# Performance work log

Hardware: AMD Instinct MI355X
Metric: run time of the kernel (lower is better)

## Reference

```python
import jax, jax.numpy as jnp
import numpy as np

B, T, DIM = 2, 2048, 1024
HEADS, DH = 16, 64
INNER = HEADS * DH
R, ALPHA = 8, 2.0
LORA_SCALE = ALPHA / R
NUM_PATCHES, NUM_FRAMES = 256, 8  # T = NUM_PATCHES*NUM_FRAMES
EPS = 1e-5


def _block_causal_mask():
    # generate_mask_matrix: frame-block causal mask [1,1,T,T]
    f = jnp.arange(T) // NUM_PATCHES
    m = (f[:, None] >= f[None, :]).astype(jnp.int32)
    return m[None, None]


def setup_inputs() -> dict:
    key = jax.random.key(0)
    ks = jax.random.split(key, 24)
    p = lambda k, shape: (jax.random.normal(k, shape, jnp.float32) * 0.02)
    inp = {
        "x": jax.random.normal(ks[0], (B, T, DIM), jnp.float32),
        "m_tok": jax.random.normal(ks[1], (B, T, DIM), jnp.float32),
        "norm_g": jnp.ones((DIM,), jnp.float32),
        "norm_b": jnp.zeros((DIM,), jnp.float32),
        "mnorm_g": jnp.ones((DIM,), jnp.float32),
        "mnorm_b": jnp.zeros((DIM,), jnp.float32),
        # q/k/v: base W [inner,dim], LoRA A [r,dim], B [inner,r], generator G [r,dim]
        "Wq": p(ks[2], (INNER, DIM)), "Aq": p(ks[3], (R, DIM)), "Bq": p(ks[4], (INNER, R)), "Gq": p(ks[5], (R, DIM)),
        "Wk": p(ks[6], (INNER, DIM)), "Ak": p(ks[7], (R, DIM)), "Bk": p(ks[8], (INNER, R)), "Gk": p(ks[9], (R, DIM)),
        "Wv": p(ks[10], (INNER, DIM)), "Av": p(ks[11], (R, DIM)), "Bv": p(ks[12], (INNER, R)), "Gv": p(ks[13], (R, DIM)),
        # o: in=inner, out=dim, mem_features=dim
        "Wo": p(ks[14], (DIM, INNER)), "Ao": p(ks[15], (R, INNER)), "Bo": p(ks[16], (DIM, R)), "Go": p(ks[17], (R, DIM)),
        "mask": _block_causal_mask(),
    }
    return inp


def _ln(x, g, b):
    mu = jnp.mean(x, -1, keepdims=True)
    var = jnp.mean(jnp.square(x - mu), -1, keepdims=True)
    return (x - mu) * jax.lax.rsqrt(var + EPS) * g + b


def _dyn_lora(x, m, W, A, Bm, G):
    # per-token dynamic LoRA: base Wx + (alpha/r) * B @ ((A x) * (G m))
    base = jnp.einsum('btd,od->bto', x, W)
    gate = jnp.einsum('btm,rm->btr', m, G)   # per-token r-dim modulation from memory token
    low = jnp.einsum('btd,rd->btr', x, A) * gate
    return base + LORA_SCALE * jnp.einsum('btr,or->bto', low, Bm)


def reference(x, m_tok, norm_g, norm_b, mnorm_g, mnorm_b,
              Wq, Aq, Bq, Gq, Wk, Ak, Bk, Gk, Wv, Av, Bv, Gv,
              Wo, Ao, Bo, Go, mask):
    xn = _ln(x, norm_g, norm_b)
    mn = _ln(m_tok, mnorm_g, mnorm_b)
    q = _dyn_lora(xn, mn, Wq, Aq, Bq, Gq).reshape(B, T, HEADS, DH)
    k = _dyn_lora(xn, mn, Wk, Ak, Bk, Gk).reshape(B, T, HEADS, DH)
    v = _dyn_lora(xn, mn, Wv, Av, Bv, Gv).reshape(B, T, HEADS, DH)
    scale = DH ** -0.5
    dots = jnp.einsum('bihd,bjhd->bhij', q, k) * scale
    dots = jnp.where(mask[:, :, :T, :T] == 0, -jnp.inf, dots)
    attn = jax.nn.softmax(dots, axis=-1)
    out = jnp.einsum('bhij,bjhd->bihd', attn, v).reshape(B, T, INNER)
    return _dyn_lora(out, mn, Wo, Ao, Bo, Go)
```

## Files before the change

### kernel.cpp

```cpp
#include <hip/hip_runtime.h>
#include <hip/hip_bf16.h>
#include <stdint.h>

typedef __bf16 bf16;
typedef bf16 bfx4 __attribute__((ext_vector_type(4)));
typedef bf16 bfx8 __attribute__((ext_vector_type(8)));
typedef __attribute__((ext_vector_type(8))) short frag_t;
typedef __attribute__((ext_vector_type(4))) float f32x4;

#define NTOK 4096
#define LORA_SCALE_F 0.25f

#define TM 128
#define TN 64

__device__ __forceinline__ bool probe_bf16(const void* ng) {
  return *(const uint32_t*)ng == 0x3F803F80u;
}
__device__ __forceinline__ float4 load4(const void* p, int idx4, bool bf) {
  if (bf) {
    bfx4 v = ((const bfx4*)p)[idx4];
    return make_float4((float)v[0], (float)v[1], (float)v[2], (float)v[3]);
  }
  return ((const float4*)p)[idx4];
}
__device__ __forceinline__ float loadf(const void* p, int i, bool bf) {
  return bf ? (float)((const bf16*)p)[i] : ((const float*)p)[i];
}

__device__ __forceinline__ int mask_type(const void* m) {
  const uint32_t w = *(const uint32_t*)m;
  if (w == 0x3F800000u) return 1;
  if (w == 0x3F803F80u) return 2;
  return 0;
}
__device__ __forceinline__ bool mask_on(const void* m, size_t idx, int mt) {
  if (mt == 0) return ((const int*)m)[idx] != 0;
  if (mt == 1) return ((const float*)m)[idx] != 0.f;
  return ((const uint16_t*)m)[idx] != 0;
}

__device__ __forceinline__ uint32_t pkbf(float a, float b) {
  union { bf16 h; unsigned short u; } x, y;
  x.h = (bf16)a; y.h = (bf16)b;
  return (uint32_t)x.u | ((uint32_t)y.u << 16);
}

__global__ __launch_bounds__(256) void verify_kernel(const void* x, const void* mt, const void* ng,
                                                     const void* Wq, const void* mask, float* flag) {
  __shared__ int sc[3];
  const int tid = threadIdx.x;
  if (tid < 3) sc[tid] = 0;
  __syncthreads();
  const bool bf = probe_bf16(ng);
  int lx = 0, lm = 0, lw = 0;
  for (int i = tid; i < 1024; i += 256) {
    if (__builtin_fabsf(loadf(x, i, bf)) > 0.25f) lx++;
    if (__builtin_fabsf(loadf(mt, i, bf)) > 0.25f) lm++;
    if (__builtin_fabsf(loadf(Wq, i, bf)) > 0.25f) lw++;
  }
  if (lx) atomicAdd(&sc[0], lx);
  if (lm) atomicAdd(&sc[1], lm);
  if (lw) atomicAdd(&sc[2], lw);
  __syncthreads();
  if (tid != 0) return;
  int code = 0;
  const uint32_t w0 = *(const uint32_t*)mask;
  int mtp = -1;
  if (w0 == 1u) mtp = 0;
  else if (w0 == 0x3F800000u) mtp = 1;
  else if (w0 == 0x3F803F80u) mtp = 2;
  if (mtp < 0) code = 30;
  if (!code && mask_on(mask, 2047, mtp)) code = 35;
  if (!code && !mask_on(mask, (size_t)2047 * 2048, mtp)) code = 36;
  if (!code) {
    for (int i = 0; i < 8 && !code; ++i) {
      uint32_t w = ((const uint32_t*)ng)[i];
      if (bf ? (w != 0x3F803F80u) : (w != 0x3F800000u)) code = 31;
    }
  }
  if (!code) {
    if (sc[0] < 600) code = 32;
    else if (sc[1] < 600) code = 33;
    else if (sc[2] > 0) code = 34;
  }
  *flag = (float)code;
}

__global__ __launch_bounds__(256) void maskchk_kernel(const void* mask, float* flag) {
  const int mt = mask_type(mask);
  const int i = blockIdx.x;
  bool bad = false;
  for (int j = threadIdx.x; j < 2048; j += 256) {
    const bool on = mask_on(mask, (size_t)i * 2048 + j, mt);
    const bool expect = (i >> 8) >= (j >> 8);
    if (on != expect) bad = true;
  }
  if (bad) *flag = 37.f;
}

__global__ void setflag_kernel(float* flag, float v) {
  if (threadIdx.x == 0 && blockIdx.x == 0) *flag = v;
}

__global__ __launch_bounds__(256) void finalize_kernel(const float* flag, float* out, int n) {
  const float f = *flag;
  if (f == 0.f) return;
  int i = (blockIdx.x * 256 + threadIdx.x) * 4;
  if (i + 3 < n) { out[i] = f; out[i + 1] = f; out[i + 2] = f; out[i + 3] = f; }
}

__global__ __launch_bounds__(256) void gates_kernel(
    const void* __restrict__ x, const void* __restrict__ mt,
    const void* __restrict__ ng, const void* __restrict__ nb,
    const void* __restrict__ mg, const void* __restrict__ mb,
    const void* __restrict__ Aq, const void* __restrict__ Ak, const void* __restrict__ Av,
    const void* __restrict__ Gq, const void* __restrict__ Gk, const void* __restrict__ Gv,
    const void* __restrict__ Go,
    float* __restrict__ lowq, float* __restrict__ lowk, float* __restrict__ lowv,
    float* __restrict__ gog, float* __restrict__ muX, float* __restrict__ rsX) {
  const bool bf = probe_bf16(ng);
  const int t = blockIdx.x;
  __shared__ float xr[1024], mr[1024];
  __shared__ float red[16];
  __shared__ float dots[56];
  const int tid = threadIdx.x, lane = tid & 63, wave = tid >> 6;
  float4 xv = load4(x, t * 256 + tid, bf);
  float4 mv = load4(mt, t * 256 + tid, bf);
  float xa[4] = {xv.x, xv.y, xv.z, xv.w};
  float ma[4] = {mv.x, mv.y, mv.z, mv.w};
  float sx = 0.f, sx2 = 0.f, sm = 0.f, sm2 = 0.f;
#pragma unroll
  for (int i = 0; i < 4; ++i) {
    sx += xa[i]; sx2 += xa[i] * xa[i];
    sm += ma[i]; sm2 += ma[i] * ma[i];
  }
#pragma unroll
  for (int d = 1; d < 64; d <<= 1) {
    sx += __shfl_xor(sx, d); sx2 += __shfl_xor(sx2, d);
    sm += __shfl_xor(sm, d); sm2 += __shfl_xor(sm2, d);
  }
  if (lane == 0) { red[wave] = sx; red[4 + wave] = sx2; red[8 + wave] = sm; red[12 + wave] = sm2; }
  __syncthreads();
  sx = red[0] + red[1] + red[2] + red[3];
  sx2 = red[4] + red[5] + red[6] + red[7];
  sm = red[8] + red[9] + red[10] + red[11];
  sm2 = red[12] + red[13] + red[14] + red[15];
  const float mux = sx * (1.f / 1024.f);
  const float rstdx = rsqrtf(sx2 * (1.f / 1024.f) - mux * mux + 1e-5f);
  const float mum = sm * (1.f / 1024.f);
  const float rstdm = rsqrtf(sm2 * (1.f / 1024.f) - mum * mum + 1e-5f);
  if (tid == 0) { muX[t] = mux; rsX[t] = rstdx; }
  float4 gx = load4(ng, tid, bf), bx = load4(nb, tid, bf);
  float4 gm = load4(mg, tid, bf), bm2 = load4(mb, tid, bf);
  float gxa[4] = {gx.x, gx.y, gx.z, gx.w}, bxa[4] = {bx.x, bx.y, bx.z, bx.w};
  float gma[4] = {gm.x, gm.y, gm.z, gm.w}, bma[4] = {bm2.x, bm2.y, bm2.z, bm2.w};
#pragma unroll
  for (int i = 0; i < 4; ++i) {
    xr[tid * 4 + i] = (xa[i] - mux) * rstdx * gxa[i] + bxa[i];
    mr[tid * 4 + i] = (ma[i] - mum) * rstdm * gma[i] + bma[i];
  }
  __syncthreads();
  const void* mats[7] = {Aq, Ak, Av, Gq, Gk, Gv, Go};
  for (int dd = wave * 14; dd < wave * 14 + 14; ++dd) {
    const int mi = dd >> 3, r = dd & 7;
    const void* M = mats[mi];
    const float* vec = (mi < 3) ? xr : mr;
    float p = 0.f;
#pragma unroll
    for (int j = 0; j < 16; ++j) {
      int idx = lane + 64 * j;
      p += vec[idx] * loadf(M, r * 1024 + idx, bf);
    }
#pragma unroll
    for (int d = 1; d < 64; d <<= 1) p += __shfl_xor(p, d);
    if (lane == 0) dots[dd] = p;
  }
  __syncthreads();
  if (tid < 8) {
    const int r = tid;
    lowq[(size_t)t * 8 + r] = dots[r] * dots[24 + r];
    lowk[(size_t)t * 8 + r] = dots[8 + r] * dots[32 + r];
    lowv[(size_t)t * 8 + r] = dots[16 + r] * dots[40 + r];
    gog[(size_t)t * 8 + r] = dots[48 + r];
  }
}

struct GemmArgs {
  const void* X;
  const float* mu;
  const float* rs;
  const void* g;
  const void* b;
  int xF32;
  int doLN;
  const void* W[3];
  const float* low[3];
  const void* Bm[3];
  void* out[3];
  int mode[3];
  float osc[3];
};

__global__ __launch_bounds__(256, 2) void proj_mfma_kernel(GemmArgs a) {
  const bool bf = probe_bf16(a.g);
  const int z = blockIdx.z;
  const int m0 = blockIdx.x * TM;
  const int n0 = blockIdx.y * TN;
  const void* __restrict__ W = a.W[z];
  __shared__ __align__(16) bf16 Xh[128][32];
  __shared__ __align__(16) bf16 Xl[128][32];
  __shared__ __align__(16) bf16 Wh[64][32];
  __shared__ __align__(16) bf16 Wl[64][32];
  __shared__ __align__(16) float lowSf[TM * 8];
  __shared__ __align__(16) float Bsf[TN * 8];
  const int tid = threadIdx.x;
  const int lane = tid & 63, wv = tid >> 6;
  const int c = lane & 15, g = lane >> 4;
  const int sr = tid >> 2;
  const int oct = tid & 3;

  ((float4*)lowSf)[tid] = ((const float4*)(a.low[z] + (size_t)m0 * 8))[tid];
  for (int e = tid; e < TN * 8; e += 256) Bsf[e] = loadf(a.Bm[z], n0 * 8 + e, bf);

  const float mu0 = a.doLN ? a.mu[m0 + sr] : 0.f;
  const float rs0 = a.doLN ? a.rs[m0 + sr] : 0.f;
  const float mu1 = a.doLN ? a.mu[m0 + sr + 64] : 0.f;
  const float rs1 = a.doLN ? a.rs[m0 + sr + 64] : 0.f;

  f32x4 acc[2][4];
#pragma unroll
  for (int mt = 0; mt < 2; ++mt)
#pragma unroll
    for (int nt = 0; nt < 4; ++nt) acc[mt][nt] = (f32x4){0.f, 0.f, 0.f, 0.f};

  for (int kt = 0; kt < 32; ++kt) {
    float4 g4a, g4b, b4a, b4b;
    if (a.doLN) {
      g4a = load4(a.g, kt * 8 + oct * 2, bf);
      g4b = load4(a.g, kt * 8 + oct * 2 + 1, bf);
      b4a = load4(a.b, kt * 8 + oct * 2, bf);
      b4b = load4(a.b, kt * 8 + oct * 2 + 1, bf);
    }
#pragma unroll
    for (int half = 0; half < 2; ++half) {
      const int row = sr + half * 64;
      const float mu = half ? mu1 : mu0;
      const float rs = half ? rs1 : rs0;
      float4 v0 = a.xF32 ? ((const float4*)a.X)[(size_t)(m0 + row) * 256 + kt * 8 + oct * 2]
                         : load4(a.X, (m0 + row) * 256 + kt * 8 + oct * 2, bf);
      float4 v1 = a.xF32 ? ((const float4*)a.X)[(size_t)(m0 + row) * 256 + kt * 8 + oct * 2 + 1]
                         : load4(a.X, (m0 + row) * 256 + kt * 8 + oct * 2 + 1, bf);
      if (a.doLN) {
        v0.x = (v0.x - mu) * rs * g4a.x + b4a.x;
        v0.y = (v0.y - mu) * rs * g4a.y + b4a.y;
        v0.z = (v0.z - mu) * rs * g4a.z + b4a.z;
        v0.w = (v0.w - mu) * rs * g4a.w + b4a.w;
        v1.x = (v1.x - mu) * rs * g4b.x + b4b.x;
        v1.y = (v1.y - mu) * rs * g4b.y + b4b.y;
        v1.z = (v1.z - mu) * rs * g4b.z + b4b.z;
        v1.w = (v1.w - mu) * rs * g4b.w + b4b.w;
      }
      float xv[8] = {v0.x, v0.y, v0.z, v0.w, v1.x, v1.y, v1.z, v1.w};
      bfx8 h8, l8;
#pragma unroll
      for (int i = 0; i < 8; ++i) {
        const bf16 hh = (bf16)xv[i];
        h8[i] = hh;
        l8[i] = (bf16)(xv[i] - (float)hh);
      }
      *(bfx8*)&Xh[row][oct * 8] = h8;
      *(bfx8*)&Xl[row][oct * 8] = l8;
    }
    {
      float4 v0 = load4(W, (n0 + sr) * 256 + kt * 8 + oct * 2, bf);
      float4 v1 = load4(W, (n0 + sr) * 256 + kt * 8 + oct * 2 + 1, bf);
      float wvv[8] = {v0.x, v0.y, v0.z, v0.w, v1.x, v1.y, v1.z, v1.w};
      bfx8 h8, l8;
#pragma unroll
      for (int i = 0; i < 8; ++i) {
        const bf16 hh = (bf16)wvv[i];
        h8[i] = hh;
        l8[i] = (bf16)(wvv[i] - (float)hh);
      }
      *(bfx8*)&Wh[sr][oct * 8] = h8;
      *(bfx8*)&Wl[sr][oct * 8] = l8;
    }
    __syncthreads();
    frag_t Ah[2], Al[2], Bh2[4], Bl2[4];
#pragma unroll
    for (int mt = 0; mt < 2; ++mt) {
      Ah[mt] = *(const frag_t*)&Xh[wv * 32 + mt * 16 + c][g * 8];
      Al[mt] = *(const frag_t*)&Xl[wv * 32 + mt * 16 + c][g * 8];
    }
#pragma unroll
    for (int nt = 0; nt < 4; ++nt) {
      Bh2[nt] = *(const frag_t*)&Wh[nt * 16 + c][g * 8];
      Bl2[nt] = *(const frag_t*)&Wl[nt * 16 + c][g * 8];
    }
#pragma unroll
    for (int mt = 0; mt < 2; ++mt)
#pragma unroll
      for (int nt = 0; nt < 4; ++nt) {
        acc[mt][nt] = __builtin_amdgcn_mfma_f32_16x16x32_bf16(Ah[mt], Bh2[nt], acc[mt][nt], 0, 0, 0);
        acc[mt][nt] = __builtin_amdgcn_mfma_f32_16x16x32_bf16(Al[mt], Bh2[nt], acc[mt][nt], 0, 0, 0);
        acc[mt][nt] = __builtin_amdgcn_mfma_f32_16x16x32_bf16(Ah[mt], Bl2[nt], acc[mt][nt], 0, 0, 0);
      }
    __syncthreads();
  }

  const float osc = a.osc[z];
  float vout[2][4][4];
#pragma unroll
  for (int mt = 0; mt < 2; ++mt)
#pragma unroll
    for (int r = 0; r < 4; ++r) {
      const int ml = wv * 32 + mt * 16 + 4 * g + r;
      const float4 la = *(const float4*)&lowSf[ml * 8];
      const float4 lb = *(const float4*)&lowSf[ml * 8 + 4];
#pragma unroll
      for (int nt = 0; nt < 4; ++nt) {
        const int nl = nt * 16 + c;
        const float4 ba = *(const float4*)&Bsf[nl * 8];
        const float4 bb = *(const float4*)&Bsf[nl * 8 + 4];
        const float add = la.x * ba.x + la.y * ba.y + la.z * ba.z + la.w * ba.w +
                          lb.x * bb.x + lb.y * bb.y + lb.z * bb.z + lb.w * bb.w;
        vout[mt][nt][r] = (acc[mt][nt][r] + LORA_SCALE_F * add) * osc;
      }
    }

  const int mode = a.mode[z];
  if (mode == 2) {
    float* o = (float*)a.out[z];
#pragma unroll
    for (int mt = 0; mt < 2; ++mt)
#pragma unroll
      for (int r = 0; r < 4; ++r) {
        const int gm = m0 + wv * 32 + mt * 16 + 4 * g + r;
#pragma unroll
        for (int nt = 0; nt < 4; ++nt)
          o[(size_t)gm * 1024 + n0 + nt * 16 + c] = vout[mt][nt][r];
      }
  } else if (mode == 1) {
    bf16* o = (bf16*)a.out[z];
    const int bb2 = m0 >> 11;
    const int h2 = n0 >> 6;
#pragma unroll
    for (int mt = 0; mt < 2; ++mt)
#pragma unroll
      for (int nt = 0; nt < 4; ++nt) {
        const int dh = nt * 16 + c;
        const int t0 = (m0 & 2047) + wv * 32 + mt * 16 + 4 * g;
        bfx4 v;
#pragma unroll
        for (int r = 0; r < 4; ++r) v[r] = (bf16)vout[mt][nt][r];
        *(bfx4*)(o + ((size_t)((bb2 * 16 + h2) * 64 + dh)) * 2048 + t0) = v;
      }
  } else {
    bf16* o = (bf16*)a.out[z];
#pragma unroll
    for (int mt = 0; mt < 2; ++mt)
#pragma unroll
      for (int r = 0; r < 4; ++r) {
        const int gm = m0 + wv * 32 + mt * 16 + 4 * g + r;
#pragma unroll
        for (int nt = 0; nt < 4; ++nt)
          o[(size_t)gm * 1024 + n0 + nt * 16 + c] = (bf16)vout[mt][nt][r];
      }
  }
}

__global__ __launch_bounds__(256, 2) void attn_mfma_kernel(
    const bf16* __restrict__ q, const bf16* __restrict__ k,
    const bf16* __restrict__ vT, float* __restrict__ attOut) {
  const int bh = blockIdx.y, b = bh >> 4, h = bh & 15;
  const int q0 = (gridDim.x - 1 - blockIdx.x) * 64;
  const int tid = threadIdx.x;
  const int wave = tid >> 6, lane = tid & 63;
  const int c = lane & 15, g = lane >> 4;
  const int c7 = c & 7;
  const int qw = q0 + wave * 16;
  const int jmax = ((q0 >> 8) + 1) << 8;

  __shared__ __align__(16) bf16 Kt[2][512 * 8];
  __shared__ __align__(16) bf16 Vt[2][512 * 8];

  const int r0 = tid >> 3, r1 = (tid + 256) >> 3;
  const int ch0 = (tid & 7) ^ (r0 & 7);
  const int ch1 = (tid & 7) ^ (r1 & 7);

  const bf16* kbh = k + ((size_t)(b * 2048)) * 1024 + h * 64;
  const bf16* vbh = vT + ((size_t)bh * 64) * 2048;
  const size_t kOff0 = (size_t)r0 * 1024 + ch0 * 8;
  const size_t kOff1 = (size_t)r1 * 1024 + ch1 * 8;
  const size_t vOff0 = (size_t)r0 * 2048 + ch0 * 8;
  const size_t vOff1 = (size_t)r1 * 2048 + ch1 * 8;

  const bf16* qbase = q + ((size_t)(b * 2048 + qw + c)) * 1024 + h * 64;
  const frag_t Bq0 = *(const frag_t*)(qbase + g * 8);
  const frag_t Bq1 = *(const frag_t*)(qbase + 32 + g * 8);

  f32x4 O[4];
#pragma unroll
  for (int dt = 0; dt < 4; ++dt) O[dt] = (f32x4){0.f, 0.f, 0.f, 0.f};
  float l_run = 0.f;

  const bool ghi = (g >> 1) != 0;
  const int s0 = ((2 * (g & 1)) << 4) | c;
  const int s1 = s0 + 16;

  bfx8 sK0 = *(const bfx8*)(kbh + kOff0);
  bfx8 sK1 = *(const bfx8*)(kbh + kOff1);
  bfx8 sV0 = *(const bfx8*)(vbh + vOff0);
  bfx8 sV1 = *(const bfx8*)(vbh + vOff1);
  *(bfx8*)&Kt[0][tid * 8] = sK0;
  *(bfx8*)&Kt[0][(tid + 256) * 8] = sK1;
  *(bfx8*)&Vt[0][tid * 8] = sV0;
  *(bfx8*)&Vt[0][(tid + 256) * 8] = sV1;

  int cur = 0;
  for (int j0 = 0; j0 < jmax; j0 += 64) {
    const bool more = (j0 + 64) < jmax;
    if (more) {
      sK0 = *(const bfx8*)(kbh + (size_t)(j0 + 64) * 1024 + kOff0);
      sK1 = *(const bfx8*)(kbh + (size_t)(j0 + 64) * 1024 + kOff1);
      sV0 = *(const bfx8*)(vbh + (j0 + 64) + vOff0);
      sV1 = *(const bfx8*)(vbh + (j0 + 64) + vOff1);
    }
    __syncthreads();
    f32x4 S[4];
#pragma unroll
    for (int jt = 0; jt < 4; ++jt) {
      const int rr = jt * 16 + c;
      const frag_t Ka0 = *(const frag_t*)&Kt[cur][(rr * 8 + (g ^ c7)) * 8];
      const frag_t Ka1 = *(const frag_t*)&Kt[cur][(rr * 8 + ((g + 4) ^ c7)) * 8];
      f32x4 sa = (f32x4){0.f, 0.f, 0.f, 0.f};
      sa = __builtin_amdgcn_mfma_f32_16x16x32_bf16(Ka0, Bq0, sa, 0, 0, 0);
      sa = __builtin_amdgcn_mfma_f32_16x16x32_bf16(Ka1, Bq1, sa, 0, 0, 0);
      S[jt] = sa;
    }
    float p[4][4];
    float psum = 0.f;
#pragma unroll
    for (int jt = 0; jt < 4; ++jt)
#pragma unroll
      for (int r = 0; r < 4; ++r) {
        p[jt][r] = __expf(S[jt][r]);
        psum += p[jt][r];
      }
    l_run += psum;
    const uint32_t dw0a = pkbf(p[0][0], p[0][1]), dw0b = pkbf(p[0][2], p[0][3]);
    const uint32_t dw1a = pkbf(p[1][0], p[1][1]), dw1b = pkbf(p[1][2], p[1][3]);
    const uint32_t dw2a = pkbf(p[2][0], p[2][1]), dw2b = pkbf(p[2][2], p[2][3]);
    const uint32_t dw3a = pkbf(p[3][0], p[3][1]), dw3b = pkbf(p[3][2], p[3][3]);
    union { frag_t s; uint32_t d[4]; } pa0, pa1;
    {
      const uint32_t l0 = (uint32_t)__shfl((int)dw0a, s0), h0 = (uint32_t)__shfl((int)dw1a, s0);
      const uint32_t l1 = (uint32_t)__shfl((int)dw0b, s0), h1 = (uint32_t)__shfl((int)dw1b, s0);
      const uint32_t l2 = (uint32_t)__shfl((int)dw0a, s1), h2 = (uint32_t)__shfl((int)dw1a, s1);
      const uint32_t l3 = (uint32_t)__shfl((int)dw0b, s1), h3 = (uint32_t)__shfl((int)dw1b, s1);
      pa0.d[0] = ghi ? h0 : l0;
      pa0.d[1] = ghi ? h1 : l1;
      pa0.d[2] = ghi ? h2 : l2;
      pa0.d[3] = ghi ? h3 : l3;
    }
    {
      const uint32_t l0 = (uint32_t)__shfl((int)dw2a, s0), h0 = (uint32_t)__shfl((int)dw3a, s0);
      const uint32_t l1 = (uint32_t)__shfl((int)dw2b, s0), h1 = (uint32_t)__shfl((int)dw3b, s0);
      const uint32_t l2 = (uint32_t)__shfl((int)dw2a, s1), h2 = (uint32_t)__shfl((int)dw3a, s1);
      const uint32_t l3 = (uint32_t)__shfl((int)dw2b, s1), h3 = (uint32_t)__shfl((int)dw3b, s1);
      pa1.d[0] = ghi ? h0 : l0;
      pa1.d[1] = ghi ? h1 : l1;
      pa1.d[2] = ghi ? h2 : l2;
      pa1.d[3] = ghi ? h3 : l3;
    }
#pragma unroll
    for (int dt = 0; dt < 4; ++dt) {
      const int vr = dt * 16 + c;
      const frag_t Vb0 = *(const frag_t*)&Vt[cur][(vr * 8 + (g ^ c7)) * 8];
      const frag_t Vb1 = *(const frag_t*)&Vt[cur][(vr * 8 + ((g + 4) ^ c7)) * 8];
      O[dt] = __builtin_amdgcn_mfma_f32_16x16x32_bf16(pa0.s, Vb0, O[dt], 0, 0, 0);
      O[dt] = __builtin_amdgcn_mfma_f32_16x16x32_bf16(pa1.s, Vb1, O[dt], 0, 0, 0);
    }
    __syncthreads();
    if (more) {
      *(bfx8*)&Kt[cur ^ 1][tid * 8] = sK0;
      *(bfx8*)&Kt[cur ^ 1][(tid + 256) * 8] = sK1;
      *(bfx8*)&Vt[cur ^ 1][tid * 8] = sV0;
      *(bfx8*)&Vt[cur ^ 1][(tid + 256) * 8] = sV1;
    }
    cur ^= 1;
  }

  l_run += __shfl_xor(l_run, 16);
  l_run += __shfl_xor(l_run, 32);
  const float inv = 1.f / l_run;
  const float i0 = __shfl(inv, 4 * g + 0);
  const float i1 = __shfl(inv, 4 * g + 1);
  const float i2 = __shfl(inv, 4 * g + 2);
  const float i3 = __shfl(inv, 4 * g + 3);
#pragma unroll
  for (int dt = 0; dt < 4; ++dt) {
    O[dt][0] *= i0; O[dt][1] *= i1; O[dt][2] *= i2; O[dt][3] *= i3;
  }
#pragma unroll
  for (int r = 0; r < 4; ++r) {
    float* orow = attOut + ((size_t)(b * 2048 + qw + 4 * g + r)) * 1024 + h * 64 + c;
#pragma unroll
    for (int dt = 0; dt < 4; ++dt) orow[dt * 16] = O[dt][r];
  }
}

__global__ __launch_bounds__(256) void lowo_kernel(
    const float* __restrict__ att, const void* __restrict__ Ao,
    const void* __restrict__ probe, const float* __restrict__ gog,
    float* __restrict__ lowo) {
  const bool bf = probe_bf16(probe);
  const int t = blockIdx.x;
  __shared__ float xr[1024];
  __shared__ float dots[8];
  const int tid = threadIdx.x, lane = tid & 63, wave = tid >> 6;
  {
    float4 a = ((const float4*)(att + (size_t)t * 1024))[tid];
    xr[tid * 4 + 0] = a.x; xr[tid * 4 + 1] = a.y;
    xr[tid * 4 + 2] = a.z; xr[tid * 4 + 3] = a.w;
  }
  __syncthreads();
  for (int dd = wave * 2; dd < wave * 2 + 2; ++dd) {
    float p = 0.f;
#pragma unroll
    for (int j = 0; j < 16; ++j) {
      int idx = lane + 64 * j;
      p += xr[idx] * loadf(Ao, dd * 1024 + idx, bf);
    }
#pragma unroll
    for (int d = 1; d < 64; d <<= 1) p += __shfl_xor(p, d);
    if (lane == 0) dots[dd] = p;
  }
  __syncthreads();
  if (tid < 8) lowo[(size_t)t * 8 + tid] = dots[tid] * gog[(size_t)t * 8 + tid];
}

__global__ __launch_bounds__(256) void copy_kernel(const float4* __restrict__ src,
                                                   float4* __restrict__ dst, int n4) {
  const int i = blockIdx.x * 256 + threadIdx.x;
  if (i < n4) dst[i] = src[i];
}

extern "C" void kernel_launch(void* const* d_in, const int* in_sizes, int n_in,
                              void* d_out, int out_size, void* d_ws, size_t ws_size,
                              hipStream_t stream) {
  float* outp = (float*)d_out;
  char* ws = (char*)d_ws;
  float* flag = (float*)(ws + (960 << 10));
  const int fin_blocks = (out_size + 1023) / 1024;

  static const unsigned char pdict[23] = {3,3,0,0,0,0, 2,1,1,1, 2,1,1,1, 2,1,1,1, 2,1,1,1, 3};
  static const unsigned char psort[23] = {1,1,1,1,1,1,1,1,1,1,1,1, 2,2,2,2, 3,3, 0,0,0,0, 3};
  int mode = -1;
  int diag = 0;
  int cls[23];
  if (n_in != 23) {
    diag = 240 + (n_in < 0 ? 0 : (n_in > 15 ? 15 : n_in));
  } else {
    long long m = 0x7FFFFFFFFFFFFFFFLL;
    bool good = true;
    for (int i = 0; i < 23; ++i) {
      if (in_sizes[i] <= 0) { good = false; break; }
      if (in_sizes[i] < m) m = in_sizes[i];
    }
    if (!good) diag = 230;
    else {
      bool cg = true;
      for (int i = 0; i < 23; ++i) {
        long long r = in_sizes[i] / m;
        cls[i] = (r == 1) ? 0 : (r == 8) ? 1 : (r == 1024) ? 2 : (r == 4096) ? 3 : 4;
        if (cls[i] == 4 || (in_sizes[i] % m) != 0) cg = false;
      }
      bool dm = cg, sm = cg, rm = cg;
      if (cg) {
        for (int i = 0; i < 23; ++i) {
          if (cls[i] != pdict[i]) dm = false;
          if (cls[i] != psort[i]) sm = false;
          if (cls[i] != pdict[22 - i]) rm = false;
        }
      }
      mode = dm ? 0 : sm ? 1 : rm ? 2 : -1;
      if (mode < 0) diag = 100 + cls[0] * 25 + cls[1] * 5 + cls[6];
    }
  }
  if (mode < 0) {
    setflag_kernel<<<1, 64, 0, stream>>>(flag, (float)diag);
    finalize_kernel<<<fin_blocks, 256, 0, stream>>>(flag, outp, out_size);
    return;
  }
  if (ws_size < ((size_t)26 << 20)) {
    setflag_kernel<<<1, 64, 0, stream>>>(flag, 25.f);
    finalize_kernel<<<fin_blocks, 256, 0, stream>>>(flag, outp, out_size);
    return;
  }

  const void* in[23];
  if (mode == 0) {
    for (int i = 0; i < 23; ++i) in[i] = d_in[i];
  } else if (mode == 1) {
    static const int perm[23] = {
        22, 16, 21, 20, 19, 18,
        14, 2, 6, 10,
        12, 0, 4, 8,
        15, 3, 7, 11,
        13, 1, 5, 9,
        17};
    for (int i = 0; i < 23; ++i) in[i] = d_in[perm[i]];
  } else {
    for (int i = 0; i < 23; ++i) in[i] = d_in[22 - i];
  }
  const void* x   = in[0];
  const void* mt  = in[1];
  const void* ng  = in[2];
  const void* nb  = in[3];
  const void* mng = in[4];
  const void* mnb = in[5];
  const void* Wq = in[6];  const void* Aq = in[7];
  const void* Bq = in[8];  const void* Gq = in[9];
  const void* Wk = in[10]; const void* Ak = in[11];
  const void* Bk = in[12]; const void* Gk = in[13];
  const void* Wv = in[14]; const void* Av = in[15];
  const void* Bv = in[16]; const void* Gv = in[17];
  const void* Wo = in[18]; const void* Ao = in[19];
  const void* Bo = in[20]; const void* Go = in[21];
  const void* mask = in[22];

  float* lowq = (float*)(ws);
  float* lowk = (float*)(ws + (128 << 10));
  float* lowv = (float*)(ws + (256 << 10));
  float* gog  = (float*)(ws + (384 << 10));
  float* lowo = (float*)(ws + (512 << 10));
  float* muX  = (float*)(ws + (640 << 10));
  float* rsX  = (float*)(ws + (704 << 10));
  bf16* qb = (bf16*)(ws + ((size_t)1 << 20));
  bf16* kb = (bf16*)(ws + ((size_t)9 << 20));
  bf16* vb = (bf16*)(ws + ((size_t)17 << 20));
  float* att = outp;
  float* oout = (float*)(ws + ((size_t)1 << 20));

  verify_kernel<<<1, 256, 0, stream>>>(x, mt, ng, Wq, mask, flag);
  maskchk_kernel<<<2048, 256, 0, stream>>>(mask, flag);

  gates_kernel<<<NTOK, 256, 0, stream>>>(x, mt, ng, nb, mng, mnb,
                                         Aq, Ak, Av, Gq, Gk, Gv, Go,
                                         lowq, lowk, lowv, gog, muX, rsX);

  GemmArgs ga;
  ga.X = x; ga.mu = muX; ga.rs = rsX; ga.g = ng; ga.b = nb;
  ga.xF32 = 0; ga.doLN = 1;
  ga.W[0] = Wq;  ga.W[1] = Wk;  ga.W[2] = Wv;
  ga.low[0] = lowq; ga.low[1] = lowk; ga.low[2] = lowv;
  ga.Bm[0] = Bq; ga.Bm[1] = Bk; ga.Bm[2] = Bv;
  ga.out[0] = qb; ga.out[1] = kb; ga.out[2] = vb;
  ga.mode[0] = 0; ga.mode[1] = 0; ga.mode[2] = 1;
  ga.osc[0] = 0.125f; ga.osc[1] = 1.f; ga.osc[2] = 1.f;
  proj_mfma_kernel<<<dim3(NTOK / TM, 1024 / TN, 3), 256, 0, stream>>>(ga);

  attn_mfma_kernel<<<dim3(32, 32), 256, 0, stream>>>(qb, kb, vb, att);

  lowo_kernel<<<NTOK, 256, 0, stream>>>(att, Ao, ng, gog, lowo);

  GemmArgs go2;
  go2.X = att; go2.mu = muX; go2.rs = rsX; go2.g = ng; go2.b = nb;
  go2.xF32 = 1; go2.doLN = 0;
  go2.W[0] = Wo; go2.W[1] = Wo; go2.W[2] = Wo;
  go2.low[0] = lowo; go2.low[1] = lowo; go2.low[2] = lowo;
  go2.Bm[0] = Bo; go2.Bm[1] = Bo; go2.Bm[2] = Bo;
  go2.out[0] = oout; go2.out[1] = oout; go2.out[2] = oout;
  go2.mode[0] = 2; go2.mode[1] = 2; go2.mode[2] = 2;
  go2.osc[0] = 1.f; go2.osc[1] = 1.f; go2.osc[2] = 1.f;
  proj_mfma_kernel<<<dim3(NTOK / TM, 1024 / TN, 1), 256, 0, stream>>>(go2);

  copy_kernel<<<NTOK, 256, 0, stream>>>((const float4*)oout, (float4*)outp, NTOK * 256);

  finalize_kernel<<<fin_blocks, 256, 0, stream>>>(flag, outp, out_size);
}
```

Baseline: 493.1 us.

## Fuse Q/K/V projections into one block sharing the LayerNorm X tile, add LDS swizzle

The QKV projection kernel now processes all three weight matrices in one block instead of launching a z-dimension of 3. The normalized and hi/lo-split X tile is built once per k-step and reused for Q, K and V, which removes two of the three redundant loads, LayerNorm passes and bf16 splits of X. LDS writes and reads also get an XOR swizzle to reduce bank conflicts. In exchange the accumulator array triples (96 floats per thread) and LDS use grows, which can cut occupancy below the launch-bounds target of 2 blocks, and the grid has a third as many blocks.

```diff
diff --git a/kernel.cpp b/kernel.cpp
--- a/kernel.cpp
+++ b/kernel.cpp
@@ -194,6 +194,7 @@
   const void* b;
   int xF32;
   int doLN;
+  int zn;
   const void* W[3];
   const float* low[3];
   const void* Bm[3];
@@ -204,35 +205,40 @@
 
 __global__ __launch_bounds__(256, 2) void proj_mfma_kernel(GemmArgs a) {
   const bool bf = probe_bf16(a.g);
-  const int z = blockIdx.z;
   const int m0 = blockIdx.x * TM;
   const int n0 = blockIdx.y * TN;
-  const void* __restrict__ W = a.W[z];
+  const int zn = a.zn;
   __shared__ __align__(16) bf16 Xh[128][32];
   __shared__ __align__(16) bf16 Xl[128][32];
-  __shared__ __align__(16) bf16 Wh[64][32];
-  __shared__ __align__(16) bf16 Wl[64][32];
-  __shared__ __align__(16) float lowSf[TM * 8];
-  __shared__ __align__(16) float Bsf[TN * 8];
+  __shared__ __align__(16) bf16 Wh[3][64][32];
+  __shared__ __align__(16) bf16 Wl[3][64][32];
+  __shared__ __align__(16) float lowSf[3][TM * 8];
+  __shared__ __align__(16) float Bsf[3][TN * 8];
   const int tid = threadIdx.x;
   const int lane = tid & 63, wv = tid >> 6;
   const int c = lane & 15, g = lane >> 4;
   const int sr = tid >> 2;
   const int oct = tid & 3;
-
-  ((float4*)lowSf)[tid] = ((const float4*)(a.low[z] + (size_t)m0 * 8))[tid];
-  for (int e = tid; e < TN * 8; e += 256) Bsf[e] = loadf(a.Bm[z], n0 * 8 + e, bf);
+  const int swS = (sr >> 1) & 3;
+  const int swR = (c >> 1) & 3;
+
+  for (int z = 0; z < zn; ++z) {
+    ((float4*)lowSf[z])[tid] = ((const float4*)(a.low[z] + (size_t)m0 * 8))[tid];
+    for (int e = tid; e < TN * 8; e += 256) Bsf[z][e] = loadf(a.Bm[z], n0 * 8 + e, bf);
+  }
 
   const float mu0 = a.doLN ? a.mu[m0 + sr] : 0.f;
   const float rs0 = a.doLN ? a.rs[m0 + sr] : 0.f;
   const float mu1 = a.doLN ? a.mu[m0 + sr + 64] : 0.f;
   const float rs1 = a.doLN ? a.rs[m0 + sr + 64] : 0.f;
 
-  f32x4 acc[2][4];
-#pragma unroll
-  for (int mt = 0; mt < 2; ++mt)
-#pragma unroll
-    for (int nt = 0; nt < 4; ++nt) acc[mt][nt] = (f32x4){0.f, 0.f, 0.f, 0.f};
+  f32x4 acc[3][2][4];
+#pragma unroll
+  for (int z = 0; z < 3; ++z)
+#pragma unroll
+    for (int mt = 0; mt < 2; ++mt)
+#pragma unroll
+      for (int nt = 0; nt < 4; ++nt) acc[z][mt][nt] = (f32x4){0.f, 0.f, 0.f, 0.f};
 
   for (int kt = 0; kt < 32; ++kt) {
     float4 g4a, g4b, b4a, b4b;
@@ -269,12 +275,12 @@
         h8[i] = hh;
         l8[i] = (bf16)(xv[i] - (float)hh);
       }
-      *(bfx8*)&Xh[row][oct * 8] = h8;
-      *(bfx8*)&Xl[row][oct * 8] = l8;
-    }
-    {
-      float4 v0 = load4(W, (n0 + sr) * 256 + kt * 8 + oct * 2, bf);
-      float4 v1 = load4(W, (n0 + sr) * 256 + kt * 8 + oct * 2 + 1, bf);
+      *(bfx8*)&Xh[row][(oct ^ swS) * 8] = h8;
+      *(bfx8*)&Xl[row][(oct ^ swS) * 8] = l8;
+    }
+    for (int z = 0; z < zn; ++z) {
+      float4 v0 = load4(a.W[z], (n0 + sr) * 256 + kt * 8 + oct * 2, bf);
+      float4 v1 = load4(a.W[z], (n0 + sr) * 256 + kt * 8 + oct * 2 + 1, bf);
       float wvv[8] = {v0.x, v0.y, v0.z, v0.w, v1.x, v1.y, v1.z, v1.w};
       bfx8 h8, l8;
 #pragma unroll
@@ -283,90 +289,94 @@
         h8[i] = hh;
         l8[i] = (bf16)(wvv[i] - (float)hh);
       }
-      *(bfx8*)&Wh[sr][oct * 8] = h8;
-      *(bfx8*)&Wl[sr][oct * 8] = l8;
+      *(bfx8*)&Wh[z][sr][(oct ^ swS) * 8] = h8;
+      *(bfx8*)&Wl[z][sr][(oct ^ swS) * 8] = l8;
     }
     __syncthreads();
-    frag_t Ah[2], Al[2], Bh2[4], Bl2[4];
+    frag_t Ah[2], Al[2];
 #pragma unroll
     for (int mt = 0; mt < 2; ++mt) {
-      Ah[mt] = *(const frag_t*)&Xh[wv * 32 + mt * 16 + c][g * 8];
-      Al[mt] = *(const frag_t*)&Xl[wv * 32 + mt * 16 + c][g * 8];
-    }
-#pragma unroll
-    for (int nt = 0; nt < 4; ++nt) {
-      Bh2[nt] = *(const frag_t*)&Wh[nt * 16 + c][g * 8];
-      Bl2[nt] = *(const frag_t*)&Wl[nt * 16 + c][g * 8];
-    }
+      Ah[mt] = *(const frag_t*)&Xh[wv * 32 + mt * 16 + c][(g ^ swR) * 8];
+      Al[mt] = *(const frag_t*)&Xl[wv * 32 + mt * 16 + c][(g ^ swR) * 8];
+    }
+    for (int z = 0; z < zn; ++z) {
+      frag_t Bh2[4], Bl2[4];
+#pragma unroll
+      for (int nt = 0; nt < 4; ++nt) {
+        Bh2[nt] = *(const frag_t*)&Wh[z][nt * 16 + c][(g ^ swR) * 8];
+        Bl2[nt] = *(const frag_t*)&Wl[z][nt * 16 + c][(g ^ swR) * 8];
+      }
+#pragma unroll
+      for (int mt = 0; mt < 2; ++mt)
+#pragma unroll
+        for (int nt = 0; nt < 4; ++nt) {
+          acc[z][mt][nt] = __builtin_amdgcn_mfma_f32_16x16x32_bf16(Ah[mt], Bh2[nt], acc[z][mt][nt], 0, 0, 0);
+          acc[z][mt][nt] = __builtin_amdgcn_mfma_f32_16x16x32_bf16(Al[mt], Bh2[nt], acc[z][mt][nt], 0, 0, 0);
+          acc[z][mt][nt] = __builtin_amdgcn_mfma_f32_16x16x32_bf16(Ah[mt], Bl2[nt], acc[z][mt][nt], 0, 0, 0);
+        }
+    }
+    __syncthreads();
+  }
+
+  for (int z = 0; z < zn; ++z) {
+    const float osc = a.osc[z];
+    const int mode = a.mode[z];
+    float vout[2][4][4];
 #pragma unroll
     for (int mt = 0; mt < 2; ++mt)
 #pragma unroll
-      for (int nt = 0; nt < 4; ++nt) {
-        acc[mt][nt] = __builtin_amdgcn_mfma_f32_16x16x32_bf16(Ah[mt], Bh2[nt], acc[mt][nt], 0, 0, 0);
-        acc[mt][nt] = __builtin_amdgcn_mfma_f32_16x16x32_bf16(Al[mt], Bh2[nt], acc[mt][nt], 0, 0, 0);
-        acc[mt][nt] = __builtin_amdgcn_mfma_f32_16x16x32_bf16(Ah[mt], Bl2[nt], acc[mt][nt], 0, 0, 0);
-      }
-    __syncthreads();
-  }
-
-  const float osc = a.osc[z];
-  float vout[2][4][4];
-#pragma unroll
-  for (int mt = 0; mt < 2; ++mt)
-#pragma unroll
-    for (int r = 0; r < 4; ++r) {
-      const int ml = wv * 32 + mt * 16 + 4 * g + r;
-      const float4 la = *(const float4*)&lowSf[ml * 8];
-      const float4 lb = *(const float4*)&lowSf[ml * 8 + 4];
-#pragma unroll
-      for (int nt = 0; nt < 4; ++nt) {
-        const int nl = nt * 16 + c;
-        const float4 ba = *(const float4*)&Bsf[nl * 8];
-        const float4 bb = *(const float4*)&Bsf[nl * 8 + 4];
-        const float add = la.x * ba.x + la.y * ba.y + la.z * ba.z + la.w * ba.w +
-                          lb.x * bb.x + lb.y * bb.y + lb.z * bb.z + lb.w * bb.w;
-        vout[mt][nt][r] = (acc[mt][nt][r] + LORA_SCALE_F * add) * osc;
-      }
-    }
-
-  const int mode = a.mode[z];
-  if (mode == 2) {
-    float* o = (float*)a.out[z];
-#pragma unroll
-    for (int mt = 0; mt < 2; ++mt)
-#pragma unroll
       for (int r = 0; r < 4; ++r) {
-        const int gm = m0 + wv * 32 + mt * 16 + 4 * g + r;
-#pragma unroll
-        for (int nt = 0; nt < 4; ++nt)
-          o[(size_t)gm * 1024 + n0 + nt * 16 + c] = vout[mt][nt][r];
-      }
-  } else if (mode == 1) {
-    bf16* o = (bf16*)a.out[z];
-    const int bb2 = m0 >> 11;
-    const int h2 = n0 >> 6;
-#pragma unroll
-    for (int mt = 0; mt < 2; ++mt)
-#pragma unroll
-      for (int nt = 0; nt < 4; ++nt) {
-        const int dh = nt * 16 + c;
-        const int t0 = (m0 & 2047) + wv * 32 + mt * 16 + 4 * g;
-        bfx4 v;
-#pragma unroll
-        for (int r = 0; r < 4; ++r) v[r] = (bf16)vout[mt][nt][r];
-        *(bfx4*)(o + ((size_t)((bb2 * 16 + h2) * 64 + dh)) * 2048 + t0) = v;
-      }
-  } else {
-    bf16* o = (bf16*)a.out[z];
-#pragma unroll
-    for (int mt = 0; mt < 2; ++mt)
-#pragma unroll
-      for (int r = 0; r < 4; ++r) {
-        const int gm = m0 + wv * 32 + mt * 16 + 4 * g + r;
-#pragma unroll
-        for (int nt = 0; nt < 4; ++nt)
-          o[(size_t)gm * 1024 + n0 + nt * 16 + c] = (bf16)vout[mt][nt][r];
-      }
+        const int ml = wv * 32 + mt * 16 + 4 * g + r;
+        const float4 la = *(const float4*)&lowSf[z][ml * 8];
+        const float4 lb = *(const float4*)&lowSf[z][ml * 8 + 4];
+#pragma unroll
+        for (int nt = 0; nt < 4; ++nt) {
+          const int nl = nt * 16 + c;
+          const float4 ba = *(const float4*)&Bsf[z][nl * 8];
+          const float4 bb = *(const float4*)&Bsf[z][nl * 8 + 4];
+          const float add = la.x * ba.x + la.y * ba.y + la.z * ba.z + la.w * ba.w +
+                            lb.x * bb.x + lb.y * bb.y + lb.z * bb.z + lb.w * bb.w;
+          vout[mt][nt][r] = (acc[z][mt][nt][r] + LORA_SCALE_F * add) * osc;
+        }
+      }
+    if (mode == 2) {
+      float* o = (float*)a.out[z];
+#pragma unroll
+      for (int mt = 0; mt < 2; ++mt)
+#pragma unroll
+        for (int r = 0; r < 4; ++r) {
+          const int gm = m0 + wv * 32 + mt * 16 + 4 * g + r;
+#pragma unroll
+          for (int nt = 0; nt < 4; ++nt)
+            o[(size_t)gm * 1024 + n0 + nt * 16 + c] = vout[mt][nt][r];
+        }
+    } else if (mode == 1) {
+      bf16* o = (bf16*)a.out[z];
+      const int bb2 = m0 >> 11;
+      const int h2 = n0 >> 6;
+#pragma unroll
+      for (int mt = 0; mt < 2; ++mt)
+#pragma unroll
+        for (int nt = 0; nt < 4; ++nt) {
+          const int dh = nt * 16 + c;
+          const int t0 = (m0 & 2047) + wv * 32 + mt * 16 + 4 * g;
+          bfx4 v;
+#pragma unroll
+          for (int r = 0; r < 4; ++r) v[r] = (bf16)vout[mt][nt][r];
+          *(bfx4*)(o + ((size_t)((bb2 * 16 + h2) * 64 + dh)) * 2048 + t0) = v;
+        }
+    } else {
+      bf16* o = (bf16*)a.out[z];
+#pragma unroll
+      for (int mt = 0; mt < 2; ++mt)
+#pragma unroll
+        for (int r = 0; r < 4; ++r) {
+          const int gm = m0 + wv * 32 + mt * 16 + 4 * g + r;
+#pragma unroll
+          for (int nt = 0; nt < 4; ++nt)
+            o[(size_t)gm * 1024 + n0 + nt * 16 + c] = (bf16)vout[mt][nt][r];
+        }
+    }
   }
 }
 
@@ -653,14 +663,14 @@
 
   GemmArgs ga;
   ga.X = x; ga.mu = muX; ga.rs = rsX; ga.g = ng; ga.b = nb;
-  ga.xF32 = 0; ga.doLN = 1;
+  ga.xF32 = 0; ga.doLN = 1; ga.zn = 3;
   ga.W[0] = Wq;  ga.W[1] = Wk;  ga.W[2] = Wv;
   ga.low[0] = lowq; ga.low[1] = lowk; ga.low[2] = lowv;
   ga.Bm[0] = Bq; ga.Bm[1] = Bk; ga.Bm[2] = Bv;
   ga.out[0] = qb; ga.out[1] = kb; ga.out[2] = vb;
   ga.mode[0] = 0; ga.mode[1] = 0; ga.mode[2] = 1;
   ga.osc[0] = 0.125f; ga.osc[1] = 1.f; ga.osc[2] = 1.f;
-  proj_mfma_kernel<<<dim3(NTOK / TM, 1024 / TN, 3), 256, 0, stream>>>(ga);
+  proj_mfma_kernel<<<dim3(NTOK / TM, 1024 / TN, 1), 256, 0, stream>>>(ga);
 
   attn_mfma_kernel<<<dim3(32, 32), 256, 0, stream>>>(qb, kb, vb, att);
 
@@ -668,7 +678,7 @@
 
   GemmArgs go2;
   go2.X = att; go2.mu = muX; go2.rs = rsX; go2.g = ng; go2.b = nb;
-  go2.xF32 = 1; go2.doLN = 0;
+  go2.xF32 = 1; go2.doLN = 0; go2.zn = 1;
   go2.W[0] = Wo; go2.W[1] = Wo; go2.W[2] = Wo;
   go2.low[0] = lowo; go2.low[1] = lowo; go2.low[2] = lowo;
   go2.Bm[0] = Bo; go2.Bm[1] = Bo; go2.Bm[2] = Bo;
```

After: 1.048 ms. +112.5%, slower.
